# Optimization experiments

Hardware: AMD Instinct MI355X
Metric: run time of the kernel (lower is better)

Reference implementation:

```python
import jax, jax.numpy as jnp
import numpy as np

K_NEIGHBORS = 1  # self.K + self.J = 1 + 0
FP_H = 56        # sqrt(args.fp_nums) = sqrt(3136)


def setup_inputs() -> dict:
    key = jax.random.key(0)
    k1, k2 = jax.random.split(key)
    embeds = jax.random.normal(k1, (32, 3136, 1024), dtype=jnp.float32)
    centroids = jax.random.normal(k2, (2048, 1024), dtype=jnp.float32)
    return {"embeds": embeds, "centroids": centroids}


def reference(embeds, centroids):
    # embeds: [B, N, D]; centroids: [M, D]
    B, N, D = embeds.shape
    # squared L2 distance via ||e||^2 + ||c||^2 - 2 e.c  (same expansion as torch code)
    feat_sq = jnp.sum(embeds * embeds, axis=2, keepdims=True)          # [B, N, 1]
    cent_sq = jnp.sum(centroids * centroids, axis=1)[None, None, :]    # [1, 1, M]
    cross = jnp.einsum('bnd,md->bnm', embeds, centroids)               # [B, N, M]
    d2 = feat_sq + cent_sq - 2.0 * cross
    # clamp tiny negative fp error before sqrt (torch sqrt would NaN there)
    dist = jnp.sqrt(jnp.maximum(d2, 0.0))                              # [B, N, M]
    # k smallest distances (ascending), k = K + J = 1
    neg_top, _ = jax.lax.top_k(-dist, K_NEIGHBORS)
    d_top = -neg_top                                                   # [B, N, k]
    # softmin over the k neighbors, weight the nearest distance
    sim = jax.nn.softmax(-d_top, axis=-1)[:, :, 0] * d_top[:, :, 0]    # [B, N]
    # rearrange 'b (h w) c -> b c h w' with c = 1
    score = sim.reshape(B, FP_H, FP_H)[:, None, :, :]                  # [B, 1, 56, 56]
    # eval mode: loss = 0; embeds is passed through unchanged, so return score
    return score
```

## Files before the change

### kernel.cpp

```cpp
#include <hip/hip_runtime.h>
#include <hip/hip_bf16.h>


typedef __bf16 bf16x8 __attribute__((ext_vector_type(8)));
typedef __bf16 bf16x4 __attribute__((ext_vector_type(4)));
typedef float f32x4 __attribute__((ext_vector_type(4)));
typedef long lx2 __attribute__((ext_vector_type(2)));

#define N_ROWS 100352
#define M_CENT 2048
#define D_K 1024

#define BM4 128
#define BN4 128
#define BK4 128
#define NT4 (D_K / BK4)
#define NCT4 (M_CENT / BN4)
#define NBLK4 ((N_ROWS / BM4) * NCT4)
#define BPX4 (NBLK4 / 8)

#define TM 128
#define TN 128
#define BK 64
#define NT_TILES (M_CENT / TN)
#define KT_STEPS (D_K / BK)

#define AS1 __attribute__((address_space(1)))
#define AS3 __attribute__((address_space(3)))

#define WAITVM(N) asm volatile("s_waitcnt vmcnt(" #N ")" ::: "memory")
#define LGKM0 asm volatile("s_waitcnt lgkmcnt(0)" ::: "memory")
#define FENCE asm volatile("" ::: "memory")

__global__ __launch_bounds__(256) void rowsq_fp8pack(const float* __restrict__ src,
                                                     unsigned char* __restrict__ dst,
                                                     float* __restrict__ sq) {
  const int m = blockIdx.x;
  const int t = threadIdx.x;
  const float4 v = *reinterpret_cast<const float4*>(src + (size_t)m * D_K + t * 4);
  int pk = __builtin_amdgcn_cvt_pk_fp8_f32(v.x, v.y, 0, false);
  pk = __builtin_amdgcn_cvt_pk_fp8_f32(v.z, v.w, pk, true);
  const int k = t * 4;
  const int seg = k >> 7;
  const int ksi = (k >> 5) & 3;
  const int g = (k >> 3) & 3;
  const int j = k & 7;
  const int p = seg * 128 + (((ksi >> 1) * 4 + g) << 4) + (ksi & 1) * 8 + j;
  *reinterpret_cast<unsigned int*>(dst + (size_t)m * D_K + p) = (unsigned int)pk;
  float ss = v.x * v.x + v.y * v.y + v.z * v.z + v.w * v.w;
  ss += __shfl_xor(ss, 1);
  ss += __shfl_xor(ss, 2);
  ss += __shfl_xor(ss, 4);
  ss += __shfl_xor(ss, 8);
  ss += __shfl_xor(ss, 16);
  ss += __shfl_xor(ss, 32);
  __shared__ float ws4[4];
  const int w = t >> 6, l = t & 63;
  if (l == 0) ws4[w] = ss;
  __syncthreads();
  if (t == 0) sq[m] = ws4[0] + ws4[1] + ws4[2] + ws4[3];
}

__global__ __launch_bounds__(256, 2) void gemm_min_fp8(const unsigned char* __restrict__ e8,
                                                       const unsigned char* __restrict__ c8,
                                                       const float* __restrict__ csq,
                                                       float* __restrict__ pmin) {
  __shared__ __align__(16) char lds[2 * 32768];
  __shared__ float rowmin2[2][BM4];

  const int t = threadIdx.x;
  const int w = t >> 6;
  const int l = t & 63;
  const int wr = w >> 1, wc = w & 1;
  const int g = l >> 4, lr = l & 15;

  const int b = blockIdx.x;
  const int swz = (b & 7) * BPX4 + (b >> 3);
  const int rp = swz >> 4, ct = swz & 15;
  const long row0 = (long)rp * BM4;
  const int col0 = ct * BN4;

  const int trow = t >> 3, tsl = t & 7;
  const int ssw = (tsl ^ (trow & 7)) << 4;
  const unsigned char* srcA0 = e8 + (row0 + trow) * (size_t)D_K + ssw;
  const unsigned char* srcB0 = c8 + (size_t)(col0 + trow) * D_K + ssw;
  const int dst0 = t * 16;

  f32x4 acc[4][4];
#pragma unroll
  for (int m = 0; m < 4; ++m)
#pragma unroll
    for (int n = 0; n < 4; ++n) acc[m][n] = (f32x4){0.f, 0.f, 0.f, 0.f};

  int offA[4][2], offB[4][2];
#pragma unroll
  for (int m = 0; m < 4; ++m) {
    const int row = wr * 64 + m * 16 + lr;
#pragma unroll
    for (int ksp = 0; ksp < 2; ++ksp)
      offA[m][ksp] = row * 128 + (((ksp * 4 + g) ^ (row & 7)) << 4);
  }
#pragma unroll
  for (int n = 0; n < 4; ++n) {
    const int col = wc * 64 + n * 16 + lr;
#pragma unroll
    for (int ksp = 0; ksp < 2; ++ksp)
      offB[n][ksp] = 16384 + col * 128 + (((ksp * 4 + g) ^ (col & 7)) << 4);
  }

  lx2 af[4][2], bfr[4][2];

  auto stage = [&](int kt, int buf) {
    char* base = lds + buf * 32768;
    const size_t ko = (size_t)kt * BK4;
#pragma unroll
    for (int i = 0; i < 4; ++i)
      __builtin_amdgcn_global_load_lds(
          (const AS1 unsigned int*)(const void*)(srcA0 + (size_t)i * 32 * D_K + ko),
          (AS3 unsigned int*)(void*)(base + i * 4096 + dst0), 16, 0, 0);
#pragma unroll
    for (int i = 0; i < 4; ++i)
      __builtin_amdgcn_global_load_lds(
          (const AS1 unsigned int*)(const void*)(srcB0 + (size_t)i * 32 * D_K + ko),
          (AS3 unsigned int*)(void*)(base + 16384 + i * 4096 + dst0), 16, 0, 0);
  };

  auto readfrags = [&](int buf) {
    const char* base = lds + buf * 32768;
#pragma unroll
    for (int m = 0; m < 4; ++m)
#pragma unroll
      for (int ksp = 0; ksp < 2; ++ksp)
        af[m][ksp] = *reinterpret_cast<const lx2*>(base + offA[m][ksp]);
#pragma unroll
    for (int n = 0; n < 4; ++n)
#pragma unroll
      for (int ksp = 0; ksp < 2; ++ksp)
        bfr[n][ksp] = *reinterpret_cast<const lx2*>(base + offB[n][ksp]);
  };

  auto domfma = [&]() {
#pragma unroll
    for (int ksp = 0; ksp < 2; ++ksp)
#pragma unroll
      for (int m = 0; m < 4; ++m)
#pragma unroll
        for (int n = 0; n < 4; ++n) {
          acc[m][n] = __builtin_amdgcn_mfma_f32_16x16x32_fp8_fp8(
              af[m][ksp][0], bfr[n][ksp][0], acc[m][n], 0, 0, 0);
          acc[m][n] = __builtin_amdgcn_mfma_f32_16x16x32_fp8_fp8(
              af[m][ksp][1], bfr[n][ksp][1], acc[m][n], 0, 0, 0);
        }
  };

  stage(0, 0);
  stage(1, 1);
#pragma unroll
  for (int kt = 0; kt < NT4; ++kt) {
    const int buf = kt & 1;
    if (kt < NT4 - 1) {
      WAITVM(8);
    } else {
      WAITVM(0);
    }
    FENCE;
    __builtin_amdgcn_s_barrier();
    FENCE;
    readfrags(buf);
    domfma();
    if (kt < NT4 - 2) {
      LGKM0;
      FENCE;
      __builtin_amdgcn_s_barrier();
      FENCE;
      stage(kt + 2, buf);
    }
  }

  float runmin[4][4];
#pragma unroll
  for (int m = 0; m < 4; ++m)
#pragma unroll
    for (int r = 0; r < 4; ++r) runmin[m][r] = 3.0e38f;
#pragma unroll
  for (int n = 0; n < 4; ++n) {
    const float cs = csq[col0 + wc * 64 + n * 16 + lr];
#pragma unroll
    for (int m = 0; m < 4; ++m)
#pragma unroll
      for (int r = 0; r < 4; ++r)
        runmin[m][r] = fminf(runmin[m][r], cs - 2.0f * acc[m][n][r]);
  }
#pragma unroll
  for (int m = 0; m < 4; ++m)
#pragma unroll
    for (int r = 0; r < 4; ++r) {
      float v = runmin[m][r];
      v = fminf(v, __shfl_xor(v, 1));
      v = fminf(v, __shfl_xor(v, 2));
      v = fminf(v, __shfl_xor(v, 4));
      v = fminf(v, __shfl_xor(v, 8));
      runmin[m][r] = v;
    }
  if (lr == 0) {
#pragma unroll
    for (int m = 0; m < 4; ++m)
#pragma unroll
      for (int r = 0; r < 4; ++r)
        rowmin2[wc][wr * 64 + m * 16 + g * 4 + r] = runmin[m][r];
  }
  __syncthreads();
  if (t < BM4) {
    pmin[(row0 + t) * NCT4 + ct] = fminf(rowmin2[0][t], rowmin2[1][t]);
  }
}

__global__ __launch_bounds__(256) void final_min(const float* __restrict__ esq,
                                                 const float* __restrict__ pmin,
                                                 float* __restrict__ out) {
  const int r = blockIdx.x * 256 + threadIdx.x;
  const float4* p = reinterpret_cast<const float4*>(pmin + (size_t)r * 16);
  float4 a = p[0], b = p[1], c = p[2], d = p[3];
  float m = fminf(fminf(fminf(a.x, a.y), fminf(a.z, a.w)),
                  fminf(fminf(b.x, b.y), fminf(b.z, b.w)));
  m = fminf(m, fminf(fminf(fminf(c.x, c.y), fminf(c.z, c.w)),
                     fminf(fminf(d.x, d.y), fminf(d.z, d.w))));
  out[r] = sqrtf(fmaxf(esq[r] + m, 0.f));
}

__global__ __launch_bounds__(256) void rowsq_bf16(const float* __restrict__ src,
                                                  __bf16* __restrict__ dst,
                                                  float* __restrict__ sq) {
  const int m = blockIdx.x;
  const int t = threadIdx.x;
  const float4 v = *reinterpret_cast<const float4*>(src + (size_t)m * D_K + t * 4);
  bf16x4 o = {(__bf16)v.x, (__bf16)v.y, (__bf16)v.z, (__bf16)v.w};
  *reinterpret_cast<bf16x4*>(dst + (size_t)m * D_K + t * 4) = o;
  float ss = v.x * v.x + v.y * v.y + v.z * v.z + v.w * v.w;
  ss += __shfl_xor(ss, 1);
  ss += __shfl_xor(ss, 2);
  ss += __shfl_xor(ss, 4);
  ss += __shfl_xor(ss, 8);
  ss += __shfl_xor(ss, 16);
  ss += __shfl_xor(ss, 32);
  __shared__ float ws4[4];
  const int w = t >> 6, l = t & 63;
  if (l == 0) ws4[w] = ss;
  __syncthreads();
  if (t == 0) sq[m] = ws4[0] + ws4[1] + ws4[2] + ws4[3];
}

template <bool WS>
__global__ __launch_bounds__(256, 2) void fused_min(const float* __restrict__ embeds,
                                                    const float* __restrict__ centf,
                                                    const __bf16* __restrict__ cbf,
                                                    const float* __restrict__ csq,
                                                    float* __restrict__ out) {
  __shared__ __align__(16) char Ab[TM * 128];
  __shared__ __align__(16) char Bb[TN * 128];
  __shared__ float rowmin2[2][TM];
  __shared__ float sqrow[TM];
  __shared__ float colsq[TN];

  const int t = threadIdx.x;
  const int w = t >> 6;
  const int l = t & 63;
  const int wr = w >> 1, wc = w & 1;
  const int g = l >> 4, lr = l & 15;
  const long row0 = (long)blockIdx.x * TM;

  float runmin[4][4];
#pragma unroll
  for (int m = 0; m < 4; ++m)
#pragma unroll
    for (int r = 0; r < 4; ++r) runmin[m][r] = 3.0e38f;

  float sqpart[8];
#pragma unroll
  for (int c = 0; c < 8; ++c) sqpart[c] = 0.f;

  for (int nt = 0; nt < NT_TILES; ++nt) {
    const int col0 = nt * TN;
    f32x4 acc[4][4];
#pragma unroll
    for (int m = 0; m < 4; ++m)
#pragma unroll
      for (int n = 0; n < 4; ++n) acc[m][n] = (f32x4){0.f, 0.f, 0.f, 0.f};

    float cpart[8];
    if constexpr (!WS) {
#pragma unroll
      for (int c = 0; c < 8; ++c) cpart[c] = 0.f;
    }

    for (int kt = 0; kt < KT_STEPS; ++kt) {
      __syncthreads();
      if constexpr (WS) {
#pragma unroll
        for (int i = 0; i < 4; ++i) {
          const int s = (w * 4 + i) * 64 + l;
          const int col = s >> 3, sl = s & 7;
          const __bf16* src =
              cbf + (size_t)(col0 + col) * D_K + kt * BK + ((sl ^ (col & 7)) << 3);
          __builtin_amdgcn_global_load_lds(
              (const AS1 unsigned int*)(const void*)src,
              (AS3 unsigned int*)(void*)(Bb + (w * 4 + i) * 1024), 16, 0, 0);
        }
      } else {
#pragma unroll
        for (int c = 0; c < 8; ++c) {
          const int f = c * 256 + t;
          const int col = f >> 4, kq = f & 15;
          const float4 v = *reinterpret_cast<const float4*>(
              centf + (size_t)(col0 + col) * D_K + kt * BK + kq * 4);
          cpart[c] += v.x * v.x + v.y * v.y + v.z * v.z + v.w * v.w;
          bf16x4 o = {(__bf16)v.x, (__bf16)v.y, (__bf16)v.z, (__bf16)v.w};
          const int slot = kq >> 1;
          *reinterpret_cast<bf16x4*>(Bb + col * 128 + ((slot ^ (col & 7)) << 4) +
                                     (kq & 1) * 8) = o;
        }
      }
#pragma unroll
      for (int c = 0; c < 8; ++c) {
        const int f = c * 256 + t;
        const int row = f >> 4, kq = f & 15;
        const float4 v = *reinterpret_cast<const float4*>(
            embeds + (row0 + row) * (long)D_K + kt * BK + kq * 4);
        if (nt == 0) sqpart[c] += v.x * v.x + v.y * v.y + v.z * v.z + v.w * v.w;
        bf16x4 o = {(__bf16)v.x, (__bf16)v.y, (__bf16)v.z, (__bf16)v.w};
        const int slot = kq >> 1;
        *reinterpret_cast<bf16x4*>(Ab + row * 128 + ((slot ^ (row & 7)) << 4) +
                                   (kq & 1) * 8) = o;
      }
      __syncthreads();
#pragma unroll
      for (int ks = 0; ks < 2; ++ks) {
        bf16x8 af[4], bfr[4];
#pragma unroll
        for (int m = 0; m < 4; ++m) {
          const int row = wr * 64 + m * 16 + lr;
          const int slot = ks * 4 + g;
          af[m] = *reinterpret_cast<const bf16x8*>(Ab + row * 128 +
                                                   ((slot ^ (row & 7)) << 4));
        }
#pragma unroll
        for (int n = 0; n < 4; ++n) {
          const int col = wc * 64 + n * 16 + lr;
          const int slot = ks * 4 + g;
          bfr[n] = *reinterpret_cast<const bf16x8*>(Bb + col * 128 +
                                                    ((slot ^ (col & 7)) << 4));
        }
#pragma unroll
        for (int m = 0; m < 4; ++m)
#pragma unroll
          for (int n = 0; n < 4; ++n)
            acc[m][n] =
                __builtin_amdgcn_mfma_f32_16x16x32_bf16(af[m], bfr[n], acc[m][n], 0, 0, 0);
      }
    }

    if (nt == 0) {
#pragma unroll
      for (int c = 0; c < 8; ++c) {
        float ss = sqpart[c];
        ss += __shfl_xor(ss, 1);
        ss += __shfl_xor(ss, 2);
        ss += __shfl_xor(ss, 4);
        ss += __shfl_xor(ss, 8);
        if (lr == 0) sqrow[c * 16 + (w * 4 + g)] = ss;
      }
    }
    if constexpr (!WS) {
#pragma unroll
      for (int c = 0; c < 8; ++c) {
        float ss = cpart[c];
        ss += __shfl_xor(ss, 1);
        ss += __shfl_xor(ss, 2);
        ss += __shfl_xor(ss, 4);
        ss += __shfl_xor(ss, 8);
        if (lr == 0) colsq[c * 16 + (w * 4 + g)] = ss;
      }
      __syncthreads();
    }

#pragma unroll
    for (int n = 0; n < 4; ++n) {
      float cs;
      if constexpr (WS)
        cs = csq[col0 + wc * 64 + n * 16 + lr];
      else
        cs = colsq[wc * 64 + n * 16 + lr];
#pragma unroll
      for (int m = 0; m < 4; ++m)
#pragma unroll
        for (int r = 0; r < 4; ++r)
          runmin[m][r] = fminf(runmin[m][r], cs - 2.0f * acc[m][n][r]);
    }
  }

#pragma unroll
  for (int m = 0; m < 4; ++m)
#pragma unroll
    for (int r = 0; r < 4; ++r) {
      float v = runmin[m][r];
      v = fminf(v, __shfl_xor(v, 1));
      v = fminf(v, __shfl_xor(v, 2));
      v = fminf(v, __shfl_xor(v, 4));
      v = fminf(v, __shfl_xor(v, 8));
      runmin[m][r] = v;
    }
  if (lr == 0) {
#pragma unroll
    for (int m = 0; m < 4; ++m)
#pragma unroll
      for (int r = 0; r < 4; ++r)
        rowmin2[wc][wr * 64 + m * 16 + g * 4 + r] = runmin[m][r];
  }
  __syncthreads();
  if (t < TM) {
    const float v = fminf(rowmin2[0][t], rowmin2[1][t]);
    out[row0 + t] = sqrtf(fmaxf(sqrow[t] + v, 0.f));
  }
}

extern "C" void kernel_launch(void* const* d_in, const int* in_sizes, int n_in,
                              void* d_out, int out_size, void* d_ws, size_t ws_size,
                              hipStream_t stream) {
  const float* embeds = (const float*)d_in[0];
  const float* cent = (const float*)d_in[1];
  float* out = (float*)d_out;

  const size_t off_c8 = 0;
  const size_t off_csq = off_c8 + (size_t)M_CENT * D_K;
  const size_t off_e8 = off_csq + (size_t)M_CENT * 4;
  const size_t off_esq = off_e8 + (size_t)N_ROWS * D_K;
  const size_t off_pmin = off_esq + (size_t)N_ROWS * 4;
  const size_t need_full = off_pmin + (size_t)N_ROWS * NCT4 * 4;
  const size_t need_small = (size_t)M_CENT * D_K * 2 + (size_t)M_CENT * 4;

  if (ws_size >= need_full) {
    unsigned char* c8 = (unsigned char*)d_ws + off_c8;
    float* csq = (float*)((char*)d_ws + off_csq);
    unsigned char* e8 = (unsigned char*)d_ws + off_e8;
    float* esq = (float*)((char*)d_ws + off_esq);
    float* pmin = (float*)((char*)d_ws + off_pmin);
    rowsq_fp8pack<<<M_CENT, 256, 0, stream>>>(cent, c8, csq);
    rowsq_fp8pack<<<N_ROWS, 256, 0, stream>>>(embeds, e8, esq);
    gemm_min_fp8<<<NBLK4, 256, 0, stream>>>(e8, c8, csq, pmin);
    final_min<<<N_ROWS / 256, 256, 0, stream>>>(esq, pmin, out);
  } else if (ws_size >= need_small) {
    __bf16* cbf = (__bf16*)d_ws;
    float* csq = (float*)((char*)d_ws + (size_t)M_CENT * D_K * 2);
    rowsq_bf16<<<M_CENT, 256, 0, stream>>>(cent, cbf, csq);
    fused_min<true><<<N_ROWS / TM, 256, 0, stream>>>(embeds, cent, cbf, csq, out);
  } else {
    fused_min<false><<<N_ROWS / TM, 256, 0, stream>>>(embeds, cent, nullptr, nullptr, out);
  }
}
```

Baseline: 398.0 us.

## Use scaled MX fp8 16x16x128 MFMA with single-buffered LDS and higher occupancy

Replaces the 16x16x32 fp8 MFMA sequence with the gfx950 scaled 16x16x128 f8f6f4 MFMA at unit scales, so each K=128 tile needs one instruction per output fragment. LDS drops from double to single buffering and launch bounds go from 2 to 4 blocks per CU, relying on occupancy rather than an in-block prefetch to hide loads. The trade-off is that each block now waits for all loads before computing, which exposes memory latency. The LDS fragment layout must also match the 128-wide operand order the new instruction expects.

```diff
diff --git a/kernel.cpp b/kernel.cpp
--- a/kernel.cpp
+++ b/kernel.cpp
@@ -5,7 +5,8 @@
 typedef __bf16 bf16x8 __attribute__((ext_vector_type(8)));
 typedef __bf16 bf16x4 __attribute__((ext_vector_type(4)));
 typedef float f32x4 __attribute__((ext_vector_type(4)));
-typedef long lx2 __attribute__((ext_vector_type(2)));
+typedef int i32x4 __attribute__((ext_vector_type(4)));
+typedef int i32x8 __attribute__((ext_vector_type(8)));
 
 #define N_ROWS 100352
 #define M_CENT 2048
@@ -61,11 +62,11 @@
   if (t == 0) sq[m] = ws4[0] + ws4[1] + ws4[2] + ws4[3];
 }
 
-__global__ __launch_bounds__(256, 2) void gemm_min_fp8(const unsigned char* __restrict__ e8,
-                                                       const unsigned char* __restrict__ c8,
-                                                       const float* __restrict__ csq,
-                                                       float* __restrict__ pmin) {
-  __shared__ __align__(16) char lds[2 * 32768];
+__global__ __launch_bounds__(256, 4) void gemm_min_mx(const unsigned char* __restrict__ e8,
+                                                      const unsigned char* __restrict__ c8,
+                                                      const float* __restrict__ csq,
+                                                      float* __restrict__ pmin) {
+  __shared__ __align__(16) char lds[32768];
   __shared__ float rowmin2[2][BM4];
 
   const int t = threadIdx.x;
@@ -108,72 +109,55 @@
       offB[n][ksp] = 16384 + col * 128 + (((ksp * 4 + g) ^ (col & 7)) << 4);
   }
 
-  lx2 af[4][2], bfr[4][2];
-
-  auto stage = [&](int kt, int buf) {
-    char* base = lds + buf * 32768;
+  auto stage = [&](int kt) {
     const size_t ko = (size_t)kt * BK4;
 #pragma unroll
     for (int i = 0; i < 4; ++i)
       __builtin_amdgcn_global_load_lds(
           (const AS1 unsigned int*)(const void*)(srcA0 + (size_t)i * 32 * D_K + ko),
-          (AS3 unsigned int*)(void*)(base + i * 4096 + dst0), 16, 0, 0);
+          (AS3 unsigned int*)(void*)(lds + i * 4096 + dst0), 16, 0, 0);
 #pragma unroll
     for (int i = 0; i < 4; ++i)
       __builtin_amdgcn_global_load_lds(
           (const AS1 unsigned int*)(const void*)(srcB0 + (size_t)i * 32 * D_K + ko),
-          (AS3 unsigned int*)(void*)(base + 16384 + i * 4096 + dst0), 16, 0, 0);
+          (AS3 unsigned int*)(void*)(lds + 16384 + i * 4096 + dst0), 16, 0, 0);
   };
 
-  auto readfrags = [&](int buf) {
-    const char* base = lds + buf * 32768;
-#pragma unroll
-    for (int m = 0; m < 4; ++m)
-#pragma unroll
-      for (int ksp = 0; ksp < 2; ++ksp)
-        af[m][ksp] = *reinterpret_cast<const lx2*>(base + offA[m][ksp]);
-#pragma unroll
-    for (int n = 0; n < 4; ++n)
-#pragma unroll
-      for (int ksp = 0; ksp < 2; ++ksp)
-        bfr[n][ksp] = *reinterpret_cast<const lx2*>(base + offB[n][ksp]);
+  auto compute_tile = [&]() {
+    i32x8 b8[4];
+#pragma unroll
+    for (int n = 0; n < 4; ++n) {
+      const i32x4 lo = *reinterpret_cast<const i32x4*>(lds + offB[n][0]);
+      const i32x4 hi = *reinterpret_cast<const i32x4*>(lds + offB[n][1]);
+      b8[n] = __builtin_shufflevector(lo, hi, 0, 1, 2, 3, 4, 5, 6, 7);
+    }
+#pragma unroll
+    for (int m = 0; m < 4; ++m) {
+      const i32x4 lo = *reinterpret_cast<const i32x4*>(lds + offA[m][0]);
+      const i32x4 hi = *reinterpret_cast<const i32x4*>(lds + offA[m][1]);
+      const i32x8 a8 = __builtin_shufflevector(lo, hi, 0, 1, 2, 3, 4, 5, 6, 7);
+#pragma unroll
+      for (int n = 0; n < 4; ++n)
+        acc[m][n] = __builtin_amdgcn_mfma_scale_f32_16x16x128_f8f6f4(
+            a8, b8[n], acc[m][n], 0 , 0 , 0, 0x7F7F7F7F, 0,
+            0x7F7F7F7F);
+    }
   };
 
-  auto domfma = [&]() {
-#pragma unroll
-    for (int ksp = 0; ksp < 2; ++ksp)
-#pragma unroll
-      for (int m = 0; m < 4; ++m)
-#pragma unroll
-        for (int n = 0; n < 4; ++n) {
-          acc[m][n] = __builtin_amdgcn_mfma_f32_16x16x32_fp8_fp8(
-              af[m][ksp][0], bfr[n][ksp][0], acc[m][n], 0, 0, 0);
-          acc[m][n] = __builtin_amdgcn_mfma_f32_16x16x32_fp8_fp8(
-              af[m][ksp][1], bfr[n][ksp][1], acc[m][n], 0, 0, 0);
-        }
-  };
-
-  stage(0, 0);
-  stage(1, 1);
+  stage(0);
 #pragma unroll
   for (int kt = 0; kt < NT4; ++kt) {
-    const int buf = kt & 1;
-    if (kt < NT4 - 1) {
-      WAITVM(8);
-    } else {
-      WAITVM(0);
-    }
+    WAITVM(0);
     FENCE;
     __builtin_amdgcn_s_barrier();
     FENCE;
-    readfrags(buf);
-    domfma();
-    if (kt < NT4 - 2) {
+    compute_tile();
+    if (kt < NT4 - 1) {
       LGKM0;
       FENCE;
       __builtin_amdgcn_s_barrier();
       FENCE;
-      stage(kt + 2, buf);
+      stage(kt + 1);
     }
   }
 
@@ -446,7 +430,7 @@
     float* pmin = (float*)((char*)d_ws + off_pmin);
     rowsq_fp8pack<<<M_CENT, 256, 0, stream>>>(cent, c8, csq);
     rowsq_fp8pack<<<N_ROWS, 256, 0, stream>>>(embeds, e8, esq);
-    gemm_min_fp8<<<NBLK4, 256, 0, stream>>>(e8, c8, csq, pmin);
+    gemm_min_mx<<<NBLK4, 256, 0, stream>>>(e8, c8, csq, pmin);
     final_min<<<N_ROWS / 256, 256, 0, stream>>>(esq, pmin, out);
   } else if (ws_size >= need_small) {
     __bf16* cbf = (__bf16*)d_ws;
```

New measurement: 416.3 us. 1.05x slower.
